# Kernel tuning notes

Hardware: AMD Instinct MI355X
Metric: run time of the kernel (lower is better)

The kernel has to match this reference:

```python
import jax, jax.numpy as jnp
import numpy as np

N_E, E_DIM = 1024, 256

def setup_inputs() -> dict:
    key = jax.random.key(0)
    kz, ke = jax.random.split(key)
    z = jax.random.normal(kz, (16, E_DIM, 64, 64), dtype=jnp.float32)
    # codebook initialized uniform(-1/n_e, 1/n_e) as in the torch module
    emb = jax.random.uniform(ke, (N_E, E_DIM), dtype=jnp.float32,
                             minval=-1.0 / N_E, maxval=1.0 / N_E)
    return {"z": z, "emb": emb}

def reference(z, emb):
    B, C, H, W = z.shape  # C == e_dim
    # NCHW -> NHWC -> [N_tokens, e_dim]
    zf = jnp.transpose(z, (0, 2, 3, 1)).reshape(-1, C)
    # squared L2 distances: ||z||^2 + ||e||^2 - 2 z.e^T  -> [N_tokens, n_e]
    d = (jnp.sum(zf * zf, axis=1, keepdims=True)
         + jnp.sum(emb * emb, axis=1)
         - 2.0 * jnp.matmul(zf, emb.T))
    idx = jnp.argmin(d, axis=1)  # [N_tokens]
    # gather codebook rows (equivalent to one-hot @ emb), back to NCHW
    z_q = jnp.take(emb, idx, axis=0).reshape(B, H, W, C)
    z_q = jnp.transpose(z_q, (0, 3, 1, 2))
    return z_q, idx[:, None]
```

## Files before the change

kernel.cpp:

```cpp
#include <hip/hip_runtime.h>
#include <hip/hip_fp16.h>
#include <math.h>

#define CDIM 256
#define NE   1024
#define HW   4096
#define NB   16
#define ZQ_SIZE (NB*CDIM*HW)

typedef unsigned short ushort_t;
typedef __attribute__((ext_vector_type(8))) _Float16 f16x8;
typedef __attribute__((ext_vector_type(8))) unsigned short u16x8;
typedef __attribute__((ext_vector_type(4))) float f32x4;

#define AS1 __attribute__((address_space(1)))
#define AS3 __attribute__((address_space(3)))

#define MARGIN 1.5e-4f

#define WS_EE    0
#define WS_ZZ    4096
#define WS_CNT   266240
#define WS_LIST  266496
#define WS_ESWZ  528640
#define WS_NEEDED 1052928

__device__ __forceinline__ float sq_nofma(float v) {
    float v2 = v * v;
    asm volatile("" : "+v"(v2));
    return v2;
}

template <typename F>
__device__ __forceinline__ float pairwise256_sq(F get) {
    float total = 0.0f;
    #pragma unroll
    for (int h = 0; h < 2; ++h) {
        float r[8];
        #pragma unroll
        for (int j = 0; j < 8; ++j) r[j] = sq_nofma(get(h * 128 + j));
        #pragma unroll
        for (int i = 8; i < 128; i += 8) {
            #pragma unroll
            for (int j = 0; j < 8; ++j) r[j] += sq_nofma(get(h * 128 + i + j));
        }
        float s = ((r[0] + r[1]) + (r[2] + r[3])) + ((r[4] + r[5]) + (r[6] + r[7]));
        total = (h == 0) ? s : (total + s);
    }
    return total;
}

template <typename F>
__device__ __forceinline__ float pairwise128_sq(F get) {
    float r[8];
    #pragma unroll
    for (int j = 0; j < 8; ++j) r[j] = sq_nofma(get(j));
    #pragma unroll
    for (int i = 8; i < 128; i += 8) {
        #pragma unroll
        for (int j = 0; j < 8; ++j) r[j] += sq_nofma(get(i + j));
    }
    return ((r[0] + r[1]) + (r[2] + r[3])) + ((r[4] + r[5]) + (r[6] + r[7]));
}

__device__ __forceinline__ ushort_t f2h(float v) {
    return __half_as_ushort(__float2half(v));
}

__global__ __launch_bounds__(256) void ee_kernel(const float* __restrict__ emb,
                                                 float* __restrict__ ee,
                                                 int* __restrict__ cnt) {
    if (blockIdx.x == 0 && threadIdx.x == 0) *cnt = 0;
    int j = blockIdx.x * 256 + threadIdx.x;
    const float* row = emb + (size_t)j * CDIM;
    ee[j] = pairwise256_sq([&](int i) { return row[i]; });
}

__global__ __launch_bounds__(256) void ecvt_kernel(const float* __restrict__ emb,
                                                   ushort_t* __restrict__ eswz,
                                                   float* __restrict__ ee,
                                                   int* __restrict__ cnt) {
    if (blockIdx.x >= 128) {
        if (blockIdx.x == 128 && threadIdx.x == 0) *cnt = 0;
        int j = (blockIdx.x - 128) * 256 + threadIdx.x;
        const float* row = emb + (size_t)j * CDIM;
        ee[j] = pairwise256_sq([&](int i) { return row[i]; });
        return;
    }
    int g = blockIdx.x * 256 + threadIdx.x;
    int s  = g >> 11;
    int r  = g & 2047;
    int cw = r >> 3;
    int kg = r & 7;
    int chunk = s >> 2, kb = s & 3;
    int f  = cw >> 4, lr = cw & 15;
    int ks = kg >> 2, lg = kg & 3;

    const float* src = emb + (size_t)(chunk * 256 + cw) * CDIM + kb * 64 + kg * 8;
    float4 a = *reinterpret_cast<const float4*>(src);
    float4 b = *reinterpret_cast<const float4*>(src + 4);
    u16x8 p = { f2h(a.x), f2h(a.y), f2h(a.z), f2h(a.w),
                f2h(b.x), f2h(b.y), f2h(b.z), f2h(b.w) };
    size_t dst = (size_t)(s * 2 + ks) * 16384 + f * 1024 + (lg * 16 + lr) * 16;
    *reinterpret_cast<u16x8*>((char*)eswz + dst) = p;
}

__global__ __launch_bounds__(512, 4) void vq_main(const float* __restrict__ z,
                                                  const float* __restrict__ emb,
                                                  const ushort_t* __restrict__ eswz,
                                                  const float* __restrict__ eew,
                                                  float* __restrict__ zzw,
                                                  int* __restrict__ cnt,
                                                  int* __restrict__ list,
                                                  float* __restrict__ out) {
    __shared__ __align__(16) char arena[70400];
    char*  zfB = arena;
    char*  esB = arena + 32768;
    float* eel = (float*)(arena + 65536);
    float* zzp = (float*)(arena + 69632);
    int*   rbj = (int*)  (arena + 70144);
    float* rd1 = (float*)(arena + 32768);
    int*   rj1 = (int*)  (arena + 33792);
    float* rd2 = (float*)(arena + 34816);

    const int tid  = threadIdx.x;
    const int lane = tid & 63;
    const int wn   = tid >> 6;
    const int hh   = wn & 1;
    const int gg   = wn >> 1;
    const int b    = blockIdx.x >> 6;
    const int hw0  = (blockIdx.x & 63) << 6;
    const float* zb = z + (size_t)b * CDIM * HW + hw0;
    const int lr = lane & 15;
    const int lg = lane >> 4;
    const int laneoff = lane << 4;

    auto issue_half = [&](int t2) {
        const char* gsrc = (const char*)eswz + (size_t)t2 * 16384;
        char* dstb = esB + ((t2 & 1) << 14);
        #pragma unroll
        for (int q = 0; q < 2; ++q)
            __builtin_amdgcn_global_load_lds(
                (const AS1 unsigned*)(gsrc + (q << 13) + (tid << 4)),
                (AS3 unsigned*)(dstb + (q << 13) + (wn << 10)), 16, 0, 0);
    };

    issue_half(0);
    issue_half(1);

    {
        const int tok = lane;
        #pragma unroll
        for (int i = 0; i < 4; ++i) {
            int kg = (wn << 2) + i;
            int k0 = kg << 3;
            u16x8 p;
            #pragma unroll
            for (int e = 0; e < 8; ++e)
                p[e] = f2h(zb[(size_t)(k0 + e) * HW + tok]);
            int m = tok >> 4, lrr = tok & 15;
            int kb_ = kg >> 3, ks_ = (kg >> 2) & 1, lg_ = kg & 3;
            int off = (((kb_ * 2 + ks_) * 4 + m) << 10) + ((lg_ * 16 + lrr) << 4);
            *(u16x8*)(zfB + off) = p;
        }
        eel[tid]       = eew[tid];
        eel[tid + 512] = eew[tid + 512];
    }
    if (tid < 128) {
        int tok = tid >> 1, h = tid & 1;
        zzp[tok * 2 + h] = pairwise128_sq([&](int i) {
            return zb[(size_t)(h * 128 + i) * HW + tok];
        });
    }
    asm volatile("s_waitcnt lgkmcnt(0)" ::: "memory");
    __builtin_amdgcn_s_barrier();

    f32x4 acc[2][4];
    float sd1[2][4], sd2[2][4];
    int   sj1[2][4];
    #pragma unroll
    for (int m = 0; m < 2; ++m)
        #pragma unroll
        for (int r = 0; r < 4; ++r) { sd1[m][r] = INFINITY; sd2[m][r] = INFINITY; sj1[m][r] = NE; }

    auto half_step = [&](int kb, int ks) {
        const char* bufc = esB + (ks << 14);
        f16x8 ah2[2], bh[4];
        #pragma unroll
        for (int m = 0; m < 2; ++m)
            ah2[m] = *(const f16x8*)(zfB + (((kb * 2 + ks) * 4 + hh * 2 + m) << 10) + laneoff);
        #pragma unroll
        for (int n = 0; n < 4; ++n)
            bh[n] = *(const f16x8*)(bufc + (((gg << 2) + n) << 10) + laneoff);
        #pragma unroll
        for (int m = 0; m < 2; ++m)
            #pragma unroll
            for (int n = 0; n < 4; ++n)
                acc[m][n] = __builtin_amdgcn_mfma_f32_16x16x32_f16(ah2[m], bh[n], acc[m][n], 0, 0, 0);
    };

    auto epilogue = [&](int chunk) {
        #pragma unroll
        for (int n = 0; n < 4; ++n) {
            int code = (chunk << 8) + (gg << 6) + (n << 4) + lr;
            float eev = eel[code];
            #pragma unroll
            for (int m = 0; m < 2; ++m)
                #pragma unroll
                for (int r = 0; r < 4; ++r) {
                    float d = eev - 2.0f * acc[m][n][r];
                    bool lt1 = d < sd1[m][r];
                    bool lt2 = d < sd2[m][r];
                    sd2[m][r] = lt1 ? sd1[m][r] : (lt2 ? d : sd2[m][r]);
                    if (lt1) { sd1[m][r] = d; sj1[m][r] = code; }
                }
        }
    };

    for (int s = 0; s < 15; ++s) {
        const int kb = s & 3;
        if (kb == 0) {
            #pragma unroll
            for (int m = 0; m < 2; ++m)
                #pragma unroll
                for (int n = 0; n < 4; ++n) acc[m][n] = (f32x4){0.f, 0.f, 0.f, 0.f};
        }
        #pragma unroll
        for (int ks = 0; ks < 2; ++ks) {
            asm volatile("s_waitcnt vmcnt(2)" ::: "memory");
            __builtin_amdgcn_s_barrier();
            half_step(kb, ks);
            asm volatile("s_waitcnt lgkmcnt(0)" ::: "memory");
            __builtin_amdgcn_s_barrier();
            issue_half(2 * s + ks + 2);
        }
        if (kb == 3) epilogue(s >> 2);
    }
    {
        asm volatile("s_waitcnt vmcnt(2)" ::: "memory");
        __builtin_amdgcn_s_barrier();
        half_step(3, 0);
        asm volatile("s_waitcnt lgkmcnt(0)" ::: "memory");
        __builtin_amdgcn_s_barrier();
        asm volatile("s_waitcnt vmcnt(0)" ::: "memory");
        __builtin_amdgcn_s_barrier();
        half_step(3, 1);
        epilogue(3);
        asm volatile("s_waitcnt lgkmcnt(0)" ::: "memory");
        __builtin_amdgcn_s_barrier();
    }

    #pragma unroll
    for (int off = 1; off <= 8; off <<= 1) {
        #pragma unroll
        for (int m = 0; m < 2; ++m)
            #pragma unroll
            for (int r = 0; r < 4; ++r) {
                float od1 = __shfl_xor(sd1[m][r], off);
                int   oj1 = __shfl_xor(sj1[m][r], off);
                float od2 = __shfl_xor(sd2[m][r], off);
                float nd2 = fminf(fmaxf(sd1[m][r], od1), fminf(sd2[m][r], od2));
                bool tk = (od1 < sd1[m][r]) || (od1 == sd1[m][r] && oj1 < sj1[m][r]);
                if (tk) { sd1[m][r] = od1; sj1[m][r] = oj1; }
                sd2[m][r] = nd2;
            }
    }
    if (lr == 0) {
        #pragma unroll
        for (int m = 0; m < 2; ++m)
            #pragma unroll
            for (int r = 0; r < 4; ++r) {
                int tok = hh * 32 + m * 16 + lg * 4 + r;
                rd1[gg * 64 + tok] = sd1[m][r];
                rj1[gg * 64 + tok] = sj1[m][r];
                rd2[gg * 64 + tok] = sd2[m][r];
            }
    }
    __syncthreads();

    if (tid < 64) {
        float d1f = rd1[tid]; int j1f = rj1[tid]; float d2f = rd2[tid];
        #pragma unroll
        for (int w = 1; w < 4; ++w) {
            float od1 = rd1[w * 64 + tid];
            int   oj1 = rj1[w * 64 + tid];
            float od2 = rd2[w * 64 + tid];
            float nd2 = fminf(fmaxf(d1f, od1), fminf(d2f, od2));
            bool tk = (od1 < d1f) || (od1 == d1f && oj1 < j1f);
            if (tk) { d1f = od1; j1f = oj1; }
            d2f = nd2;
        }
        rbj[tid] = j1f;
        int gtok = b * HW + hw0 + tid;
        out[(size_t)ZQ_SIZE + gtok] = (float)j1f;
        zzw[gtok] = zzp[2 * tid] + zzp[2 * tid + 1];
        if (!(d2f - d1f > MARGIN)) {
            int slot = atomicAdd(cnt, 1);
            list[slot] = gtok;
        }
    }
    __syncthreads();

    float* zq_st = (float*)arena;
    {
        int row = tid >> 3, sub = tid & 7;
        int j = rbj[row];
        const float* er = emb + (size_t)j * CDIM;
        #pragma unroll
        for (int i = 0; i < 8; ++i) {
            int c = (sub << 2) + (i << 5);
            float4 v = *reinterpret_cast<const float4*>(er + c);
            *reinterpret_cast<float4*>(&zq_st[row * 260 + c]) = v;
        }
    }
    __syncthreads();
    {
        int tok = tid & 63, cg = tid >> 6;
        float* ob = out + (size_t)b * CDIM * HW + hw0 + tok;
        #pragma unroll 4
        for (int i = 0; i < 32; ++i) {
            int c = (cg << 5) + i;
            ob[(size_t)c * HW] = zq_st[tok * 260 + c];
        }
    }
}

__global__ __launch_bounds__(512) void vq_fallback(const float* __restrict__ z,
                                                   const float* __restrict__ emb,
                                                   const float* __restrict__ eew,
                                                   const float* __restrict__ zzw,
                                                   const int* __restrict__ cnt,
                                                   const int* __restrict__ list,
                                                   float* __restrict__ out) {
    __shared__ __align__(16) float elds[64 * 260];
    __shared__ float zrow[8][256];
    __shared__ int   toks[8];

    const int tid  = threadIdx.x;
    const int lane = tid & 63;
    const int wv   = tid >> 6;
    const int nt   = *cnt;
    const int groups = (nt + 7) >> 3;

    for (int g = blockIdx.x; g < groups; g += gridDim.x) {
        if (tid < 8) toks[tid] = (g * 8 + tid < nt) ? list[g * 8 + tid] : -1;
        __syncthreads();
        const int gt  = toks[wv];
        const bool act = gt >= 0;
        const int tb  = act ? (gt >> 12) : 0;
        const int thw = act ? (gt & 4095) : 0;
        if (act) {
            #pragma unroll
            for (int i = 0; i < 4; ++i)
                zrow[wv][i * 64 + lane] = z[(size_t)tb * CDIM * HW + (size_t)(i * 64 + lane) * HW + thw];
        }
        const float zz = act ? zzw[gt] : 0.0f;
        float d1 = INFINITY; int j1 = NE;

        for (int c = 0; c < 16; ++c) {
            __syncthreads();
            {
                int row = tid >> 3, sub = tid & 7;
                #pragma unroll
                for (int i = 0; i < 8; ++i) {
                    int col = (sub << 2) + (i << 5);
                    float4 v = *reinterpret_cast<const float4*>(
                        &emb[(size_t)(c * 64 + row) * CDIM + col]);
                    *reinterpret_cast<float4*>(&elds[row * 260 + col]) = v;
                }
            }
            __syncthreads();
            if (act) {
                float acc = 0.0f;
                #pragma unroll 8
                for (int kq = 0; kq < 64; ++kq) {
                    float4 ev = *reinterpret_cast<const float4*>(&elds[lane * 260 + kq * 4]);
                    float4 zv = *reinterpret_cast<const float4*>(&zrow[wv][kq * 4]);
                    acc = fmaf(zv.x, ev.x, acc);
                    acc = fmaf(zv.y, ev.y, acc);
                    acc = fmaf(zv.z, ev.z, acc);
                    acc = fmaf(zv.w, ev.w, acc);
                }
                int j = c * 64 + lane;
                float t1 = zz + eew[j];
                float d  = t1 - 2.0f * acc;
                if (d < d1) { d1 = d; j1 = j; }
            }
        }
        #pragma unroll
        for (int off = 1; off <= 32; off <<= 1) {
            float od = __shfl_xor(d1, off);
            int   oj = __shfl_xor(j1, off);
            if (od < d1 || (od == d1 && oj < j1)) { d1 = od; j1 = oj; }
        }
        if (act) {
            if (lane == 0) out[(size_t)ZQ_SIZE + gt] = (float)j1;
            #pragma unroll
            for (int i = 0; i < 4; ++i) {
                int cc = i * 64 + lane;
                out[(size_t)tb * CDIM * HW + (size_t)cc * HW + thw] = emb[(size_t)j1 * CDIM + cc];
            }
        }
        __syncthreads();
    }
}

#define BM 32
#define BN 256
#define BK 16
__global__ __launch_bounds__(256, 3) void vq_legacy(const float* __restrict__ z,
                                                    const float* __restrict__ emb,
                                                    const float* __restrict__ ee,
                                                    float* __restrict__ out) {
    __shared__ float zs[CDIM][BM];
    __shared__ float es[BK][BN];
    __shared__ float ees[BN];
    __shared__ float zzs[BM];
    __shared__ float red_d[4][BM];
    __shared__ int   red_j[4][BM];
    __shared__ int   bestj_s[BM];

    const int tid = threadIdx.x;
    const int b   = blockIdx.x >> 7;
    const int hw0 = (blockIdx.x & 127) << 5;
    const int ti  = tid & 7;
    const int tj  = tid >> 3;
    const int tm0 = ti << 2;
    const int jc0 = tj << 3;
    {
        const float* zb = z + (size_t)b * CDIM * HW + hw0;
        #pragma unroll
        for (int r = 0; r < 8; ++r) {
            int f4 = (r << 8) + tid;
            int c  = f4 >> 3;
            int t4 = (f4 & 7) << 2;
            float4 v = *reinterpret_cast<const float4*>(zb + (size_t)c * HW + t4);
            *reinterpret_cast<float4*>(&zs[c][t4]) = v;
        }
    }
    __syncthreads();
    if (tid < BM) zzs[tid] = pairwise256_sq([&](int i) { return zs[i][tid]; });
    __syncthreads();
    float bd[4]; int bj[4];
    #pragma unroll
    for (int i = 0; i < 4; ++i) { bd[i] = INFINITY; bj[i] = NE; }
    for (int jt = 0; jt < NE / BN; ++jt) {
        const int j0 = jt * BN;
        float acc[4][8];
        #pragma unroll
        for (int i = 0; i < 4; ++i)
            #pragma unroll
            for (int jj = 0; jj < 8; ++jj) acc[i][jj] = 0.0f;
        for (int kt = 0; kt < CDIM / BK; ++kt) {
            __syncthreads();
            #pragma unroll
            for (int r = 0; r < 4; ++r) {
                int f4 = (r << 8) + tid;
                int jj = f4 >> 2;
                int c4 = (f4 & 3) << 2;
                float4 v = *reinterpret_cast<const float4*>(
                    emb + (size_t)(j0 + jj) * CDIM + kt * BK + c4);
                es[c4 + 0][jj] = v.x; es[c4 + 1][jj] = v.y;
                es[c4 + 2][jj] = v.z; es[c4 + 3][jj] = v.w;
            }
            if (kt == 0 && tid < BN) ees[tid] = ee[j0 + tid];
            __syncthreads();
            #pragma unroll
            for (int k = 0; k < BK; ++k) {
                float4 av  = *reinterpret_cast<const float4*>(&zs[kt * BK + k][tm0]);
                float4 bv0 = *reinterpret_cast<const float4*>(&es[k][jc0]);
                float4 bv1 = *reinterpret_cast<const float4*>(&es[k][jc0 + 4]);
                float bb[8] = {bv0.x, bv0.y, bv0.z, bv0.w, bv1.x, bv1.y, bv1.z, bv1.w};
                #pragma unroll
                for (int jj = 0; jj < 8; ++jj) {
                    acc[0][jj] = fmaf(av.x, bb[jj], acc[0][jj]);
                    acc[1][jj] = fmaf(av.y, bb[jj], acc[1][jj]);
                    acc[2][jj] = fmaf(av.z, bb[jj], acc[2][jj]);
                    acc[3][jj] = fmaf(av.w, bb[jj], acc[3][jj]);
                }
            }
        }
        #pragma unroll
        for (int i = 0; i < 4; ++i) {
            float zzv = zzs[tm0 + i];
            #pragma unroll
            for (int jj = 0; jj < 8; ++jj) {
                float t1 = zzv + ees[jc0 + jj];
                float d  = t1 - 2.0f * acc[i][jj];
                if (d < bd[i]) { bd[i] = d; bj[i] = j0 + jc0 + jj; }
            }
        }
    }
    #pragma unroll
    for (int off = 8; off <= 32; off <<= 1) {
        #pragma unroll
        for (int i = 0; i < 4; ++i) {
            float od = __shfl_xor(bd[i], off);
            int   oj = __shfl_xor(bj[i], off);
            if (od < bd[i] || (od == bd[i] && oj < bj[i])) { bd[i] = od; bj[i] = oj; }
        }
    }
    {
        const int lane = tid & 63;
        const int w    = tid >> 6;
        if (lane < 8) {
            #pragma unroll
            for (int i = 0; i < 4; ++i) {
                red_d[w][lane * 4 + i] = bd[i];
                red_j[w][lane * 4 + i] = bj[i];
            }
        }
    }
    __syncthreads();
    if (tid < BM) {
        float d = red_d[0][tid]; int j = red_j[0][tid];
        #pragma unroll
        for (int w2 = 1; w2 < 4; ++w2) {
            float od = red_d[w2][tid]; int oj = red_j[w2][tid];
            if (od < d || (od == d && oj < j)) { d = od; j = oj; }
        }
        bestj_s[tid] = j;
        out[(size_t)ZQ_SIZE + (size_t)b * HW + hw0 + tid] = (float)j;
    }
    __syncthreads();
    {
        const int t  = tid & 31;
        const int c0 = tid >> 5;
        const int jb = bestj_s[t];
        const float* er = emb + (size_t)jb * CDIM;
        float* ob = out + (size_t)b * CDIM * HW + hw0 + t;
        #pragma unroll
        for (int c = c0; c < CDIM; c += 8) ob[(size_t)c * HW] = er[c];
    }
}

extern "C" void kernel_launch(void* const* d_in, const int* in_sizes, int n_in,
                              void* d_out, int out_size, void* d_ws, size_t ws_size,
                              hipStream_t stream) {
    const float* z   = (const float*)d_in[0];
    const float* emb = (const float*)d_in[1];
    float* out = (float*)d_out;
    char*  ws  = (char*)d_ws;

    float*    ee   = (float*)(ws + WS_EE);
    float*    zzw  = (float*)(ws + WS_ZZ);
    int*      cnt  = (int*)  (ws + WS_CNT);
    int*      list = (int*)  (ws + WS_LIST);
    ushort_t* eswz = (ushort_t*)(ws + WS_ESWZ);

    if (ws_size >= (size_t)WS_NEEDED) {
        ecvt_kernel<<<dim3(132), dim3(256), 0, stream>>>(emb, eswz, ee, cnt);
        vq_main<<<dim3((NB * HW) / 64), dim3(512), 0, stream>>>(z, emb, eswz, ee, zzw,
                                                                cnt, list, out);
        vq_fallback<<<dim3(128), dim3(512), 0, stream>>>(z, emb, ee, zzw, cnt, list, out);
    } else {
        ee_kernel<<<dim3(NE / 256), dim3(256), 0, stream>>>(emb, ee, cnt);
        vq_legacy<<<dim3((NB * HW) / BM), dim3(256), 0, stream>>>(z, emb, ee, out);
    }
}
```

Baseline: 250.1 us.

## Restructure fp32 fallback rescoring into split-codebook atomicMin pass plus finalize kernel

Replaces the fallback kernel, which processed 8 ambiguous tokens per block with LDS-staged codebook tiles, with a kernel that keeps 64 tokens' z vectors in registers and has each wave scan 128 codebook rows. The two halves of the codebook go to paired blocks, which merge via a packed 64-bit atomicMin keyed on (distance, index). A separate finalize kernel then writes indices and gathered rows. The workspace region is reused for the keys and memset first, which adds two launches. A relaid-out async-load variant is also added, but it stays unused.

```diff
diff --git a/kernel.cpp b/kernel.cpp
--- a/kernel.cpp
+++ b/kernel.cpp
@@ -9,6 +9,7 @@
 #define ZQ_SIZE (NB*CDIM*HW)
 
 typedef unsigned short ushort_t;
+typedef unsigned long long u64;
 typedef __attribute__((ext_vector_type(8))) _Float16 f16x8;
 typedef __attribute__((ext_vector_type(8))) unsigned short u16x8;
 typedef __attribute__((ext_vector_type(4))) float f32x4;
@@ -68,9 +69,7 @@
 }
 
 __global__ __launch_bounds__(256) void ee_kernel(const float* __restrict__ emb,
-                                                 float* __restrict__ ee,
-                                                 int* __restrict__ cnt) {
-    if (blockIdx.x == 0 && threadIdx.x == 0) *cnt = 0;
+                                                 float* __restrict__ ee) {
     int j = blockIdx.x * 256 + threadIdx.x;
     const float* row = emb + (size_t)j * CDIM;
     ee[j] = pairwise256_sq([&](int i) { return row[i]; });
@@ -136,6 +135,16 @@
     const int laneoff = lane << 4;
 
     auto issue_half = [&](int t2) {
+        const char* gsrc = (const char*)eswz + (size_t)t2 * 16384 + (wn << 11) + laneoff;
+        char* dstb = esB + ((t2 & 1) << 14);
+        #pragma unroll
+        for (int q = 0; q < 2; ++q)
+            __builtin_amdgcn_global_load_lds(
+                (const AS1 unsigned*)(gsrc + (q << 10)),
+                (AS3 unsigned*)(dstb + (wn << 11) + (q << 10)), 16, 0, 0);
+    };
+
+    auto issue_half_r10 = [&](int t2) {
         const char* gsrc = (const char*)eswz + (size_t)t2 * 16384;
         char* dstb = esB + ((t2 & 1) << 14);
         #pragma unroll
@@ -144,9 +153,10 @@
                 (const AS1 unsigned*)(gsrc + (q << 13) + (tid << 4)),
                 (AS3 unsigned*)(dstb + (q << 13) + (wn << 10)), 16, 0, 0);
     };
-
-    issue_half(0);
-    issue_half(1);
+    (void)issue_half;
+
+    issue_half_r10(0);
+    issue_half_r10(1);
 
     {
         const int tok = lane;
@@ -232,7 +242,7 @@
             half_step(kb, ks);
             asm volatile("s_waitcnt lgkmcnt(0)" ::: "memory");
             __builtin_amdgcn_s_barrier();
-            issue_half(2 * s + ks + 2);
+            issue_half_r10(2 * s + ks + 2);
         }
         if (kb == 3) epilogue(s >> 2);
     }
@@ -325,84 +335,90 @@
     }
 }
 
-__global__ __launch_bounds__(512) void vq_fallback(const float* __restrict__ z,
-                                                   const float* __restrict__ emb,
-                                                   const float* __restrict__ eew,
-                                                   const float* __restrict__ zzw,
-                                                   const int* __restrict__ cnt,
-                                                   const int* __restrict__ list,
-                                                   float* __restrict__ out) {
-    __shared__ __align__(16) float elds[64 * 260];
-    __shared__ float zrow[8][256];
-    __shared__ int   toks[8];
-
+__global__ __launch_bounds__(256, 1) void vq_fb(const float* __restrict__ z,
+                                                const float* __restrict__ emb,
+                                                const float* __restrict__ eew,
+                                                const float* __restrict__ zzw,
+                                                const int* __restrict__ cnt,
+                                                const int* __restrict__ list,
+                                                u64* __restrict__ pk) {
+    __shared__ float zl[64][257];
     const int tid  = threadIdx.x;
     const int lane = tid & 63;
     const int wv   = tid >> 6;
+    const int half = blockIdx.x & 1;
     const int nt   = *cnt;
-    const int groups = (nt + 7) >> 3;
-
-    for (int g = blockIdx.x; g < groups; g += gridDim.x) {
-        if (tid < 8) toks[tid] = (g * 8 + tid < nt) ? list[g * 8 + tid] : -1;
+    const int gstep = gridDim.x >> 1;
+
+    for (int g = blockIdx.x >> 1; g * 64 < nt; g += gstep) {
+        {
+            int slot = tid >> 2, seg = tid & 3;
+            int li = g * 64 + slot;
+            int gt = list[(li < nt) ? li : (nt - 1)];
+            int tb = gt >> 12, thw = gt & 4095;
+            const float* zp = z + (size_t)tb * CDIM * HW + thw;
+            #pragma unroll 8
+            for (int i = 0; i < 64; ++i) {
+                int k = seg * 64 + i;
+                zl[slot][k] = zp[(size_t)k * HW];
+            }
+        }
         __syncthreads();
-        const int gt  = toks[wv];
-        const bool act = gt >= 0;
-        const int tb  = act ? (gt >> 12) : 0;
-        const int thw = act ? (gt & 4095) : 0;
+        float4 zr[64];
+        #pragma unroll
+        for (int q = 0; q < 64; ++q)
+            zr[q] = *reinterpret_cast<const float4*>(&zl[lane][q * 4]);
+
+        const int li = g * 64 + lane;
+        const bool act = li < nt;
+        const int gt = act ? list[li] : list[nt - 1];
+        const float zz = zzw[gt];
+
+        float da = INFINITY; int ja = NE;
+        const int j0 = half * 512 + wv * 128;
+        const float* eb = emb + (size_t)j0 * CDIM;
+        #pragma unroll 2
+        for (int cc = 0; cc < 128; ++cc) {
+            const float* er = eb + (size_t)cc * CDIM;
+            float acc = 0.0f;
+            #pragma unroll
+            for (int q = 0; q < 64; ++q) {
+                float4 e = *reinterpret_cast<const float4*>(er + q * 4);
+                acc = fmaf(zr[q].x, e.x, acc);
+                acc = fmaf(zr[q].y, e.y, acc);
+                acc = fmaf(zr[q].z, e.z, acc);
+                acc = fmaf(zr[q].w, e.w, acc);
+            }
+            int j = j0 + cc;
+            float t1 = zz + eew[j];
+            float d  = t1 - 2.0f * acc;
+            if (d < da) { da = d; ja = j; }
+        }
         if (act) {
-            #pragma unroll
-            for (int i = 0; i < 4; ++i)
-                zrow[wv][i * 64 + lane] = z[(size_t)tb * CDIM * HW + (size_t)(i * 64 + lane) * HW + thw];
-        }
-        const float zz = act ? zzw[gt] : 0.0f;
-        float d1 = INFINITY; int j1 = NE;
-
-        for (int c = 0; c < 16; ++c) {
-            __syncthreads();
-            {
-                int row = tid >> 3, sub = tid & 7;
-                #pragma unroll
-                for (int i = 0; i < 8; ++i) {
-                    int col = (sub << 2) + (i << 5);
-                    float4 v = *reinterpret_cast<const float4*>(
-                        &emb[(size_t)(c * 64 + row) * CDIM + col]);
-                    *reinterpret_cast<float4*>(&elds[row * 260 + col]) = v;
-                }
-            }
-            __syncthreads();
-            if (act) {
-                float acc = 0.0f;
-                #pragma unroll 8
-                for (int kq = 0; kq < 64; ++kq) {
-                    float4 ev = *reinterpret_cast<const float4*>(&elds[lane * 260 + kq * 4]);
-                    float4 zv = *reinterpret_cast<const float4*>(&zrow[wv][kq * 4]);
-                    acc = fmaf(zv.x, ev.x, acc);
-                    acc = fmaf(zv.y, ev.y, acc);
-                    acc = fmaf(zv.z, ev.z, acc);
-                    acc = fmaf(zv.w, ev.w, acc);
-                }
-                int j = c * 64 + lane;
-                float t1 = zz + eew[j];
-                float d  = t1 - 2.0f * acc;
-                if (d < d1) { d1 = d; j1 = j; }
-            }
-        }
-        #pragma unroll
-        for (int off = 1; off <= 32; off <<= 1) {
-            float od = __shfl_xor(d1, off);
-            int   oj = __shfl_xor(j1, off);
-            if (od < d1 || (od == d1 && oj < j1)) { d1 = od; j1 = oj; }
-        }
-        if (act) {
-            if (lane == 0) out[(size_t)ZQ_SIZE + gt] = (float)j1;
-            #pragma unroll
-            for (int i = 0; i < 4; ++i) {
-                int cc = i * 64 + lane;
-                out[(size_t)tb * CDIM * HW + (size_t)cc * HW + thw] = emb[(size_t)j1 * CDIM + cc];
-            }
+            u64 key = ((u64)__float_as_uint(da) << 32) | (unsigned)ja;
+            atomicMin(&pk[li], key);
         }
         __syncthreads();
     }
+}
+
+__global__ __launch_bounds__(256) void vq_fin(const float* __restrict__ emb,
+                                              const int* __restrict__ cnt,
+                                              const int* __restrict__ list,
+                                              const u64* __restrict__ pk,
+                                              float* __restrict__ out) {
+    int i = blockIdx.x * 256 + threadIdx.x;
+    if (i >= *cnt) return;
+    u64 v = pk[i];
+    int j  = (int)(v & 0xFFFFFFFFull);
+    int gt = list[i];
+    out[(size_t)ZQ_SIZE + gt] = (float)j;
+    int tb = gt >> 12, thw = gt & 4095;
+    const float* er = emb + (size_t)j * CDIM;
+    float* ob = out + (size_t)tb * CDIM * HW + thw;
+    #pragma unroll 4
+    for (int c = 0; c < CDIM; ++c)
+        ob[(size_t)c * HW] = er[c];
 }
 
 #define BM 32
@@ -547,14 +563,17 @@
     int*      cnt  = (int*)  (ws + WS_CNT);
     int*      list = (int*)  (ws + WS_LIST);
     ushort_t* eswz = (ushort_t*)(ws + WS_ESWZ);
+    u64*      pk   = (u64*)  (ws + WS_ESWZ);
 
     if (ws_size >= (size_t)WS_NEEDED) {
         ecvt_kernel<<<dim3(132), dim3(256), 0, stream>>>(emb, eswz, ee, cnt);
         vq_main<<<dim3((NB * HW) / 64), dim3(512), 0, stream>>>(z, emb, eswz, ee, zzw,
                                                                 cnt, list, out);
-        vq_fallback<<<dim3(128), dim3(512), 0, stream>>>(z, emb, ee, zzw, cnt, list, out);
+        hipMemsetAsync(pk, 0xFF, (size_t)65536 * sizeof(u64), stream);
+        vq_fb<<<dim3(128), dim3(256), 0, stream>>>(z, emb, ee, zzw, cnt, list, pk);
+        vq_fin<<<dim3(256), dim3(256), 0, stream>>>(emb, cnt, list, pk, out);
     } else {
-        ee_kernel<<<dim3(NE / 256), dim3(256), 0, stream>>>(emb, ee, cnt);
+        ee_kernel<<<dim3(NE / 256), dim3(256), 0, stream>>>(emb, ee);
         vq_legacy<<<dim3((NB * HW) / BM), dim3(256), 0, stream>>>(z, emb, ee, out);
     }
 }
```

Result: slower. 859.4 us (+243.6%).
